# Kernel optimization log

Measured on AMD Instinct MI355X. Metric: run time of the kernel, lower is better.

## Reference

```python
import jax, jax.numpy as jnp
import numpy as np

B, S, D, H, F = 16, 577, 1024, 16, 4096
DH = D // H  # 64
EPS = 1e-6


def _layernorm(x, g, b):
    mu = jnp.mean(x, axis=-1, keepdims=True)
    var = jnp.mean(jnp.square(x - mu), axis=-1, keepdims=True)
    return (x - mu) * jax.lax.rsqrt(var + EPS) * g + b


def setup_inputs() -> dict:
    key = jax.random.key(0)
    ks = jax.random.split(key, 8)
    s = 1.0 / np.sqrt(D)
    sf = 1.0 / np.sqrt(F)
    return {
        "x": jax.random.normal(ks[0], (B, S, D), jnp.float32),
        "ln1_g": jnp.ones((D,), jnp.float32),
        "ln1_b": jnp.zeros((D,), jnp.float32),
        "wq": jax.random.normal(ks[1], (D, D), jnp.float32) * s,
        "bq": jnp.zeros((D,), jnp.float32),
        "wk": jax.random.normal(ks[2], (D, D), jnp.float32) * s,
        "bk": jnp.zeros((D,), jnp.float32),
        "wv": jax.random.normal(ks[3], (D, D), jnp.float32) * s,
        "bv": jnp.zeros((D,), jnp.float32),
        "wo": jax.random.normal(ks[4], (D, D), jnp.float32) * s,
        "bo": jnp.zeros((D,), jnp.float32),
        "ln2_g": jnp.ones((D,), jnp.float32),
        "ln2_b": jnp.zeros((D,), jnp.float32),
        "w1": jax.random.normal(ks[5], (D, F), jnp.float32) * s,
        "b1": jnp.zeros((F,), jnp.float32),
        "w2": jax.random.normal(ks[6], (F, D), jnp.float32) * sf,
        "b2": jnp.zeros((D,), jnp.float32),
    }


def reference(x, ln1_g, ln1_b, wq, bq, wk, bk, wv, bv, wo, bo,
              ln2_g, ln2_b, w1, b1, w2, b2):
    # --- attention sublayer ---
    h = x
    xn = _layernorm(x, ln1_g, ln1_b)
    q = (xn @ wq + bq).reshape(B, S, H, DH).transpose(0, 2, 1, 3)  # b h s d
    k = (xn @ wk + bk).reshape(B, S, H, DH).transpose(0, 2, 1, 3)
    v = (xn @ wv + bv).reshape(B, S, H, DH).transpose(0, 2, 1, 3)
    scores = jnp.einsum('bhqd,bhkd->bhqk', q, k) / np.sqrt(DH)
    probs = jax.nn.softmax(scores, axis=-1)
    ctx = jnp.einsum('bhqk,bhkd->bhqd', probs, v)
    ctx = ctx.transpose(0, 2, 1, 3).reshape(B, S, D)
    attn_out = ctx @ wo + bo  # dropout rate 0 -> mask of ones
    x = attn_out + h
    # --- MLP sublayer ---
    h = x
    xn = _layernorm(x, ln2_g, ln2_b)
    hmid = jax.nn.gelu(xn @ w1 + b1, approximate=False)
    x = (hmid @ w2 + b2) + h
    return x
```

## Files before the change

kernel.cpp:

```cpp
#include <hip/hip_runtime.h>
#include <hip/hip_fp16.h>
#include <math.h>

#define Bn 16
#define Sn 577
#define Dn 1024
#define Hn 16
#define DHn 64
#define Fn 4096
#define NROW (Bn*Sn)
#define EPSf 1e-6f

typedef unsigned short u16;
typedef unsigned int u32;
typedef __attribute__((ext_vector_type(8))) _Float16 f16x8;
typedef __attribute__((ext_vector_type(4))) float f32x4;

__device__ inline u16 f2h(float x) { return __half_as_ushort(__float2half(x)); }

__device__ inline void xcd_swizzle(int& bx, int& by) {
    int gx = gridDim.x;
    int nwg = gx * gridDim.y;
    int n = by * gx + bx;
    if ((nwg & 7) == 0) {
        int cpx = nwg >> 3;
        int w = (n & 7) * cpx + (n >> 3);
        bx = w % gx;
        by = w / gx;
    }
}

__global__ __launch_bounds__(256) void wconv16(const float* __restrict__ W,
                                               u16* __restrict__ T16,
                                               int K, int N) {
    __shared__ float t[32][33];
    int n0 = blockIdx.x * 32, k0 = blockIdx.y * 32;
    int tx = threadIdx.x & 31, ty = threadIdx.x >> 5;
#pragma unroll
    for (int i = 0; i < 4; i++) {
        int kk = ty * 4 + i;
        t[kk][tx] = W[(size_t)(k0 + kk) * N + n0 + tx];
    }
    __syncthreads();
#pragma unroll
    for (int i = 0; i < 4; i++) {
        int nn = ty * 4 + i;
        T16[(size_t)(n0 + nn) * K + k0 + tx] = f2h(t[tx][nn]);
    }
}

__global__ __launch_bounds__(256) void ln_f16(const float* __restrict__ x,
                                              const float* __restrict__ g,
                                              const float* __restrict__ b,
                                              u16* __restrict__ oh) {
    int row = blockIdx.x;
    int tid = threadIdx.x;
    const float* xr = x + (size_t)row * Dn;
    float v[4];
    float s = 0.f;
#pragma unroll
    for (int i = 0; i < 4; i++) { v[i] = xr[tid + i * 256]; s += v[i]; }
    __shared__ float red[256];
    red[tid] = s; __syncthreads();
    for (int o = 128; o > 0; o >>= 1) { if (tid < o) red[tid] += red[tid + o]; __syncthreads(); }
    float mean = red[0] * (1.f / Dn);
    __syncthreads();
    float sq = 0.f;
#pragma unroll
    for (int i = 0; i < 4; i++) { float d = v[i] - mean; sq += d * d; }
    red[tid] = sq; __syncthreads();
    for (int o = 128; o > 0; o >>= 1) { if (tid < o) red[tid] += red[tid + o]; __syncthreads(); }
    float rstd = rsqrtf(red[0] * (1.f / Dn) + EPSf);
#pragma unroll
    for (int i = 0; i < 4; i++) {
        int c = tid + i * 256;
        float y = (v[i] - mean) * rstd * g[c] + b[c];
        oh[(size_t)row * Dn + c] = f2h(y);
    }
}

__global__ __launch_bounds__(256) void ln_kernel(const float* __restrict__ x,
                                                 const float* __restrict__ g,
                                                 const float* __restrict__ b,
                                                 float* __restrict__ out) {
    int row = blockIdx.x;
    int tid = threadIdx.x;
    const float* xr = x + (size_t)row * Dn;
    float v[4];
    float s = 0.f;
#pragma unroll
    for (int i = 0; i < 4; i++) { v[i] = xr[tid + i * 256]; s += v[i]; }
    __shared__ float red[256];
    red[tid] = s; __syncthreads();
    for (int o = 128; o > 0; o >>= 1) { if (tid < o) red[tid] += red[tid + o]; __syncthreads(); }
    float mean = red[0] * (1.f / Dn);
    __syncthreads();
    float sq = 0.f;
#pragma unroll
    for (int i = 0; i < 4; i++) { float d = v[i] - mean; sq += d * d; }
    red[tid] = sq; __syncthreads();
    for (int o = 128; o > 0; o >>= 1) { if (tid < o) red[tid] += red[tid + o]; __syncthreads(); }
    float rstd = rsqrtf(red[0] * (1.f / Dn) + EPSf);
    float* orow = out + (size_t)row * Dn;
#pragma unroll
    for (int i = 0; i < 4; i++) {
        int c = tid + i * 256;
        orow[c] = (v[i] - mean) * rstd * g[c] + b[c];
    }
}

__device__ inline void gld_lds16(const u16* g, u16* l) {
    __builtin_amdgcn_global_load_lds((const __attribute__((address_space(1))) void*)g,
                                     (__attribute__((address_space(3))) void*)l,
                                     16, 0, 0);
}

template<int EPI>
__global__ __launch_bounds__(256, 4) void gemm_1t(
    const u16* __restrict__ A, const u16* __restrict__ B,
    const float* __restrict__ bias, const float* __restrict__ resid,
    float* __restrict__ Cf, u16* __restrict__ Ch,
    int M, int N, int K)
{
    __shared__ u16 lds[2][2][4096];
    const int tid = threadIdx.x;
    const int l = tid & 63, w = tid >> 6;
    const int wr = (w >> 1) * 64, wc = (w & 1) * 64;
    int bx = blockIdx.x, by = blockIdx.y;
    xcd_swizzle(bx, by);
    const int row0 = by * 128, col0 = bx * 128;

    const int sg = w * 2;
    const int tl0 = sg * 16 + (l >> 2);
    const int tl1 = tl0 + 16;
    const int kq0 = (l & 3) ^ ((tl0 >> 1) & 3);
    const int kq1 = (l & 3) ^ ((tl1 >> 1) & 3);
    int ga0 = row0 + tl0; if (ga0 > M - 1) ga0 = M - 1;
    int ga1 = row0 + tl1; if (ga1 > M - 1) ga1 = M - 1;
    int gb0 = col0 + tl0; if (gb0 > N - 1) gb0 = N - 1;
    int gb1 = col0 + tl1; if (gb1 > N - 1) gb1 = N - 1;
    const u16* pA0 = A + (size_t)ga0 * K + kq0 * 8;
    const u16* pA1 = A + (size_t)ga1 * K + kq1 * 8;
    const u16* pB0 = B + (size_t)gb0 * K + kq0 * 8;
    const u16* pB1 = B + (size_t)gb1 * K + kq1 * 8;

    int offA[4], offB[4];
#pragma unroll
    for (int i = 0; i < 4; i++) {
        int ra = wr + i * 16 + (l & 15);
        offA[i] = ra * 32 + (((l >> 4) ^ ((ra >> 1) & 3)) << 3);
        int rb = wc + i * 16 + (l & 15);
        offB[i] = rb * 32 + (((l >> 4) ^ ((rb >> 1) & 3)) << 3);
    }

    f32x4 acc[4][4];
#pragma unroll
    for (int i = 0; i < 4; i++)
#pragma unroll
        for (int j = 0; j < 4; j++)
            acc[i][j] = (f32x4){0.f, 0.f, 0.f, 0.f};

    auto STAGE = [&](int buf, int kk) {
        gld_lds16(pA0 + kk, &lds[buf][0][(sg + 0) * 512]);
        gld_lds16(pA1 + kk, &lds[buf][0][(sg + 1) * 512]);
        gld_lds16(pB0 + kk, &lds[buf][1][(sg + 0) * 512]);
        gld_lds16(pB1 + kk, &lds[buf][1][(sg + 1) * 512]);
    };
    auto COMPUTE = [&](int buf) {
        f16x8 af[4], bf4[4];
#pragma unroll
        for (int i = 0; i < 4; i++) af[i] = *(const f16x8*)(&lds[buf][0][offA[i]]);
#pragma unroll
        for (int j = 0; j < 4; j++) bf4[j] = *(const f16x8*)(&lds[buf][1][offB[j]]);
#pragma unroll
        for (int i = 0; i < 4; i++)
#pragma unroll
            for (int j = 0; j < 4; j++)
                acc[i][j] = __builtin_amdgcn_mfma_f32_16x16x32_f16(af[i], bf4[j], acc[i][j], 0, 0, 0);
    };

    const int nk = K / 32;
    STAGE(0, 0);
    __syncthreads();
    for (int t = 0; t < nk; t += 2) {
        if (t + 1 < nk) STAGE(1, (t + 1) * 32);
        COMPUTE(0);
        __syncthreads();
        if (t + 2 < nk) STAGE(0, (t + 2) * 32);
        COMPUTE(1);
        __syncthreads();
    }

    const int rq = l >> 4;
#pragma unroll
    for (int i = 0; i < 4; i++) {
#pragma unroll
        for (int j = 0; j < 4; j++) {
            int col = col0 + wc + j * 16 + (l & 15);
            float bs = bias[col];
#pragma unroll
            for (int r = 0; r < 4; r++) {
                int rowg = row0 + wr + i * 16 + rq * 4 + r;
                if (rowg >= M) continue;
                float vv = acc[i][j][r] + bs;
                size_t o = (size_t)rowg * N + col;
                if (EPI == 1) {
                    float gl = 0.5f * vv * (1.f + erff(vv * 0.70710678118654752f));
                    Ch[o] = f2h(gl);
                } else if (EPI == 2) {
                    Cf[o] = vv + resid[o];
                } else {
                    Cf[o] = vv;
                }
            }
        }
    }
}

__global__ __launch_bounds__(256, 4) void gemm_qkv(
    const u16* __restrict__ A, const u16* __restrict__ B,
    const float* __restrict__ bq, const float* __restrict__ bk,
    const float* __restrict__ bv,
    u16* __restrict__ qb, u16* __restrict__ kb, u16* __restrict__ vt,
    int M, int N, int K)
{
    __shared__ u16 lds[2][2][4096];
    const int tid = threadIdx.x;
    const int l = tid & 63, w = tid >> 6;
    const int wr = (w >> 1) * 64, wc = (w & 1) * 64;
    int bx = blockIdx.x, by = blockIdx.y;
    xcd_swizzle(bx, by);
    const int row0 = by * 128, col0 = bx * 128;

    const int sg = w * 2;
    const int tl0 = sg * 16 + (l >> 2);
    const int tl1 = tl0 + 16;
    const int kq0 = (l & 3) ^ ((tl0 >> 1) & 3);
    const int kq1 = (l & 3) ^ ((tl1 >> 1) & 3);
    int ga0 = row0 + tl0; if (ga0 > M - 1) ga0 = M - 1;
    int ga1 = row0 + tl1; if (ga1 > M - 1) ga1 = M - 1;
    int gb0 = col0 + tl0; if (gb0 > N - 1) gb0 = N - 1;
    int gb1 = col0 + tl1; if (gb1 > N - 1) gb1 = N - 1;
    const u16* pA0 = A + (size_t)ga0 * K + kq0 * 8;
    const u16* pA1 = A + (size_t)ga1 * K + kq1 * 8;
    const u16* pB0 = B + (size_t)gb0 * K + kq0 * 8;
    const u16* pB1 = B + (size_t)gb1 * K + kq1 * 8;

    int offA[4], offB[4];
#pragma unroll
    for (int i = 0; i < 4; i++) {
        int ra = wr + i * 16 + (l & 15);
        offA[i] = ra * 32 + (((l >> 4) ^ ((ra >> 1) & 3)) << 3);
        int rb = wc + i * 16 + (l & 15);
        offB[i] = rb * 32 + (((l >> 4) ^ ((rb >> 1) & 3)) << 3);
    }

    f32x4 acc[4][4];
#pragma unroll
    for (int i = 0; i < 4; i++)
#pragma unroll
        for (int j = 0; j < 4; j++)
            acc[i][j] = (f32x4){0.f, 0.f, 0.f, 0.f};

    auto STAGE = [&](int buf, int kk) {
        gld_lds16(pA0 + kk, &lds[buf][0][(sg + 0) * 512]);
        gld_lds16(pA1 + kk, &lds[buf][0][(sg + 1) * 512]);
        gld_lds16(pB0 + kk, &lds[buf][1][(sg + 0) * 512]);
        gld_lds16(pB1 + kk, &lds[buf][1][(sg + 1) * 512]);
    };
    auto COMPUTE = [&](int buf) {
        f16x8 af[4], bf4[4];
#pragma unroll
        for (int i = 0; i < 4; i++) af[i] = *(const f16x8*)(&lds[buf][0][offA[i]]);
#pragma unroll
        for (int j = 0; j < 4; j++) bf4[j] = *(const f16x8*)(&lds[buf][1][offB[j]]);
#pragma unroll
        for (int i = 0; i < 4; i++)
#pragma unroll
            for (int j = 0; j < 4; j++)
                acc[i][j] = __builtin_amdgcn_mfma_f32_16x16x32_f16(af[i], bf4[j], acc[i][j], 0, 0, 0);
    };

    const int nk = K / 32;
    STAGE(0, 0);
    __syncthreads();
    for (int t = 0; t < nk; t += 2) {
        if (t + 1 < nk) STAGE(1, (t + 1) * 32);
        COMPUTE(0);
        __syncthreads();
        if (t + 2 < nk) STAGE(0, (t + 2) * 32);
        COMPUTE(1);
        __syncthreads();
    }

    const int rq = l >> 4;
#pragma unroll
    for (int i = 0; i < 4; i++) {
#pragma unroll
        for (int j = 0; j < 4; j++) {
            int col = col0 + wc + j * 16 + (l & 15);
#pragma unroll
            for (int r = 0; r < 4; r++) {
                int rowg = row0 + wr + i * 16 + rq * 4 + r;
                if (rowg >= M) continue;
                float a = acc[i][j][r];
                if (col < 1024) {
                    qb[(size_t)rowg * 1024 + col] = f2h((a + bq[col]) * 0.125f);
                } else if (col < 2048) {
                    int c2 = col - 1024;
                    kb[(size_t)rowg * 1024 + c2] = f2h(a + bk[c2]);
                } else {
                    int c2 = col - 2048;
                    u32 rg = (u32)rowg;
                    u32 bb = rg / 577u;
                    u32 key = rg - bb * 577u;
                    vt[((size_t)((bb * 16 + (c2 >> 6)) * 64 + (c2 & 63))) * 640 + key] =
                        f2h(a + bv[c2]);
                }
            }
        }
    }
}

__global__ __launch_bounds__(256) void flash_mfma(const u16* __restrict__ Qg,
                                                  const u16* __restrict__ Kg,
                                                  const u16* __restrict__ Vt,
                                                  u16* __restrict__ Oh) {
    __shared__ u16 Kl[64 * 64];
    __shared__ u16 Vl[64 * 64];
    __shared__ u16 Pl[64][72];

    int bx = blockIdx.x, by = blockIdx.y;
    xcd_swizzle(bx, by);
    const int qt = bx, bh = by;
    const int b = bh >> 4, h = bh & 15;
    const int tid = threadIdx.x;
    const int l = tid & 63, w = tid >> 6;
    const int q0 = qt * 64;

    int qrow = q0 + w * 16 + (l & 15); if (qrow > 576) qrow = 576;
    const u16* qp = Qg + ((size_t)(b * 577 + qrow)) * 1024 + h * 64 + (l >> 4) * 8;
    f16x8 qf0 = *(const f16x8*)qp;
    f16x8 qf1 = *(const f16x8*)(qp + 32);

    const int swk = ((l & 7) ^ (l >> 3)) * 8;

    f32x4 ctx[4];
#pragma unroll
    for (int d = 0; d < 4; d++) ctx[d] = (f32x4){0.f, 0.f, 0.f, 0.f};
    float m_r[4], l_r[4];
#pragma unroll
    for (int r = 0; r < 4; r++) { m_r[r] = -1e30f; l_r[r] = 0.f; }

    for (int kt = 0; kt < 10; ++kt) {
        const int kb = kt * 64;
#pragma unroll
        for (int c2 = 0; c2 < 2; ++c2) {
            int c = w * 2 + c2;
            int key = kb + c * 8 + (l >> 3); if (key > 576) key = 576;
            const u16* ksrc = Kg + ((size_t)(b * 577 + key)) * 1024 + h * 64 + swk;
            gld_lds16(ksrc, Kl + c * 512);
            int d = c * 8 + (l >> 3);
            const u16* vsrc = Vt + ((size_t)(bh * 64 + d)) * 640 + kb + swk;
            gld_lds16(vsrc, Vl + c * 512);
        }
        __syncthreads();

        f32x4 sc[4];
#pragma unroll
        for (int sub = 0; sub < 4; ++sub) {
            sc[sub] = (f32x4){0.f, 0.f, 0.f, 0.f};
            int rr = sub * 16 + (l & 15);
            int c0 = (l >> 4) ^ (rr & 7);
            int c1 = ((l >> 4) + 4) ^ (rr & 7);
            f16x8 kf0 = *(const f16x8*)(Kl + rr * 64 + c0 * 8);
            f16x8 kf1 = *(const f16x8*)(Kl + rr * 64 + c1 * 8);
            sc[sub] = __builtin_amdgcn_mfma_f32_16x16x32_f16(qf0, kf0, sc[sub], 0, 0, 0);
            sc[sub] = __builtin_amdgcn_mfma_f32_16x16x32_f16(qf1, kf1, sc[sub], 0, 0, 0);
        }

        bool valid[4];
#pragma unroll
        for (int sub = 0; sub < 4; ++sub) valid[sub] = (kb + sub * 16 + (l & 15)) < Sn;

#pragma unroll
        for (int r = 0; r < 4; ++r) {
            float s0 = valid[0] ? sc[0][r] : -1e30f;
            float s1 = valid[1] ? sc[1][r] : -1e30f;
            float s2 = valid[2] ? sc[2][r] : -1e30f;
            float s3 = valid[3] ? sc[3][r] : -1e30f;
            float mx = fmaxf(fmaxf(s0, s1), fmaxf(s2, s3));
            mx = fmaxf(mx, __shfl_xor(mx, 1));
            mx = fmaxf(mx, __shfl_xor(mx, 2));
            mx = fmaxf(mx, __shfl_xor(mx, 4));
            mx = fmaxf(mx, __shfl_xor(mx, 8));
            float mnew = fmaxf(m_r[r], mx);
            float scale = __expf(m_r[r] - mnew);
            float p0 = valid[0] ? __expf(s0 - mnew) : 0.f;
            float p1 = valid[1] ? __expf(s1 - mnew) : 0.f;
            float p2 = valid[2] ? __expf(s2 - mnew) : 0.f;
            float p3 = valid[3] ? __expf(s3 - mnew) : 0.f;
            int prow = w * 16 + (l >> 4) * 4 + r;
            int pcol = l & 15;
            Pl[prow][pcol]      = f2h(p0);
            Pl[prow][pcol + 16] = f2h(p1);
            Pl[prow][pcol + 32] = f2h(p2);
            Pl[prow][pcol + 48] = f2h(p3);
            float rsum = p0 + p1 + p2 + p3;
            rsum += __shfl_xor(rsum, 1);
            rsum += __shfl_xor(rsum, 2);
            rsum += __shfl_xor(rsum, 4);
            rsum += __shfl_xor(rsum, 8);
            l_r[r] = l_r[r] * scale + rsum;
            m_r[r] = mnew;
#pragma unroll
            for (int d = 0; d < 4; ++d) ctx[d][r] *= scale;
        }

#pragma unroll
        for (int ks = 0; ks < 2; ++ks) {
            f16x8 pf = *(const f16x8*)(&Pl[w * 16 + (l & 15)][ks * 32 + (l >> 4) * 8]);
#pragma unroll
            for (int d = 0; d < 4; ++d) {
                int rr = d * 16 + (l & 15);
                int cv = (ks * 4 + (l >> 4)) ^ (rr & 7);
                f16x8 vf = *(const f16x8*)(Vl + rr * 64 + cv * 8);
                ctx[d] = __builtin_amdgcn_mfma_f32_16x16x32_f16(pf, vf, ctx[d], 0, 0, 0);
            }
        }
        __syncthreads();
    }

#pragma unroll
    for (int r = 0; r < 4; ++r) {
        int q = q0 + w * 16 + (l >> 4) * 4 + r;
        if (q >= Sn) continue;
        float inv = 1.f / l_r[r];
#pragma unroll
        for (int d = 0; d < 4; ++d) {
            float t = ctx[d][r] * inv;
            size_t o = ((size_t)(b * 577 + q)) * 1024 + h * 64 + d * 16 + (l & 15);
            Oh[o] = f2h(t);
        }
    }
}

template<int EPI>
__global__ __launch_bounds__(256) void gemm_kernel(const float* __restrict__ A,
                                                   const float* __restrict__ W,
                                                   const float* __restrict__ bias,
                                                   const float* __restrict__ resid,
                                                   float* __restrict__ C,
                                                   int M, int N, int K) {
    const int BM = 64, BN = 64, BK = 16;
    __shared__ float As[BK][BM + 1];
    __shared__ float Ws[BK][BN];
    int tx = threadIdx.x, ty = threadIdx.y;
    int tid = ty * 16 + tx;
    int row0 = blockIdx.y * BM, col0 = blockIdx.x * BN;
    float acc[4][4] = {};
    for (int k0 = 0; k0 < K; k0 += BK) {
#pragma unroll
        for (int i = 0; i < 4; i++) {
            int idx = i * 256 + tid;
            int ar = idx >> 4, ac = idx & 15;
            int grow = row0 + ar;
            As[ac][ar] = (grow < M) ? A[(size_t)grow * K + k0 + ac] : 0.f;
        }
#pragma unroll
        for (int i = 0; i < 4; i++) {
            int idx = i * 256 + tid;
            int wr = idx >> 6, wcc = idx & 63;
            Ws[wr][wcc] = W[(size_t)(k0 + wr) * N + col0 + wcc];
        }
        __syncthreads();
#pragma unroll
        for (int kk = 0; kk < BK; kk++) {
            float a[4], wv[4];
#pragma unroll
            for (int i = 0; i < 4; i++) a[i] = As[kk][ty * 4 + i];
#pragma unroll
            for (int j = 0; j < 4; j++) wv[j] = Ws[kk][tx * 4 + j];
#pragma unroll
            for (int i = 0; i < 4; i++)
#pragma unroll
                for (int j = 0; j < 4; j++)
                    acc[i][j] += a[i] * wv[j];
        }
        __syncthreads();
    }
#pragma unroll
    for (int i = 0; i < 4; i++) {
        int grow = row0 + ty * 4 + i;
        if (grow >= M) continue;
#pragma unroll
        for (int j = 0; j < 4; j++) {
            int gcol = col0 + tx * 4 + j;
            float r = acc[i][j] + bias[gcol];
            if (EPI == 1) r = 0.5f * r * (1.f + erff(r * 0.70710678118654752f));
            if (EPI == 2) r += resid[(size_t)grow * N + gcol];
            C[(size_t)grow * N + gcol] = r;
        }
    }
}

__global__ __launch_bounds__(256) void flash_kernel(const float* __restrict__ Q,
                                                    const float* __restrict__ K,
                                                    const float* __restrict__ V,
                                                    float* __restrict__ Of) {
    __shared__ float Qs[64][68];
    __shared__ float KT[64][68];
    __shared__ float Vs[64][68];
    __shared__ float Ps[64][68];

    int qt = blockIdx.x;
    int bh = blockIdx.y;
    int b = bh >> 4, h = bh & 15;
    int tid = threadIdx.x;
    int tx = tid & 15, ty = tid >> 4;
    size_t base = ((size_t)b * Sn) * Dn + (size_t)h * DHn;
    int q0 = qt * 64;

    {
        int r = tid >> 4;
        int c = (tid & 15) * 4;
#pragma unroll
        for (int i = 0; i < 4; i++) {
            int rr = r + i * 16;
            int gq = q0 + rr;
            float4 val = make_float4(0.f, 0.f, 0.f, 0.f);
            if (gq < Sn) val = *(const float4*)&Q[base + (size_t)gq * Dn + c];
            Qs[rr][c + 0] = val.x * 0.125f;
            Qs[rr][c + 1] = val.y * 0.125f;
            Qs[rr][c + 2] = val.z * 0.125f;
            Qs[rr][c + 3] = val.w * 0.125f;
        }
    }

    float m_r[4], l_r[4], acc[4][4];
#pragma unroll
    for (int i = 0; i < 4; i++) {
        m_r[i] = -1e30f; l_r[i] = 0.f;
#pragma unroll
        for (int j = 0; j < 4; j++) acc[i][j] = 0.f;
    }

    for (int kt = 0; kt < 10; kt++) {
        int kb = kt * 64;
        {
            int r = tid >> 4;
            int c = (tid & 15) * 4;
#pragma unroll
            for (int i = 0; i < 4; i++) {
                int rr = r + i * 16;
                int gk = kb + rr;
                float4 kv = make_float4(0.f, 0.f, 0.f, 0.f);
                float4 vv = make_float4(0.f, 0.f, 0.f, 0.f);
                if (gk < Sn) {
                    kv = *(const float4*)&K[base + (size_t)gk * Dn + c];
                    vv = *(const float4*)&V[base + (size_t)gk * Dn + c];
                }
                KT[c + 0][rr] = kv.x;
                KT[c + 1][rr] = kv.y;
                KT[c + 2][rr] = kv.z;
                KT[c + 3][rr] = kv.w;
                Vs[rr][c + 0] = vv.x;
                Vs[rr][c + 1] = vv.y;
                Vs[rr][c + 2] = vv.z;
                Vs[rr][c + 3] = vv.w;
            }
        }
        __syncthreads();

        float s[4][4] = {};
#pragma unroll
        for (int kk4 = 0; kk4 < 16; kk4++) {
            float4 a4[4], b4[4];
#pragma unroll
            for (int i = 0; i < 4; i++) a4[i] = *(const float4*)&Qs[ty * 4 + i][kk4 * 4];
#pragma unroll
            for (int q = 0; q < 4; q++) b4[q] = *(const float4*)&KT[kk4 * 4 + q][tx * 4];
#pragma unroll
            for (int i = 0; i < 4; i++) {
                float av[4] = {a4[i].x, a4[i].y, a4[i].z, a4[i].w};
#pragma unroll
                for (int q = 0; q < 4; q++) {
                    s[i][0] += av[q] * b4[q].x;
                    s[i][1] += av[q] * b4[q].y;
                    s[i][2] += av[q] * b4[q].z;
                    s[i][3] += av[q] * b4[q].w;
                }
            }
        }

        bool cvalid[4];
#pragma unroll
        for (int j = 0; j < 4; j++) cvalid[j] = (kb + tx * 4 + j) < Sn;
#pragma unroll
        for (int i = 0; i < 4; i++) {
            float lmax = -1e30f;
#pragma unroll
            for (int j = 0; j < 4; j++) if (cvalid[j]) lmax = fmaxf(lmax, s[i][j]);
            lmax = fmaxf(lmax, __shfl_xor(lmax, 1));
            lmax = fmaxf(lmax, __shfl_xor(lmax, 2));
            lmax = fmaxf(lmax, __shfl_xor(lmax, 4));
            lmax = fmaxf(lmax, __shfl_xor(lmax, 8));
            float mnew = fmaxf(m_r[i], lmax);
            float scale = __expf(m_r[i] - mnew);
            float rsum = 0.f;
#pragma unroll
            for (int j = 0; j < 4; j++) {
                float p = cvalid[j] ? __expf(s[i][j] - mnew) : 0.f;
                s[i][j] = p;
                rsum += p;
            }
            rsum += __shfl_xor(rsum, 1);
            rsum += __shfl_xor(rsum, 2);
            rsum += __shfl_xor(rsum, 4);
            rsum += __shfl_xor(rsum, 8);
            l_r[i] = l_r[i] * scale + rsum;
            m_r[i] = mnew;
#pragma unroll
            for (int j = 0; j < 4; j++) acc[i][j] *= scale;
        }

#pragma unroll
        for (int i = 0; i < 4; i++)
#pragma unroll
            for (int j = 0; j < 4; j++)
                Ps[ty * 4 + i][tx * 4 + j] = s[i][j];
        __syncthreads();

#pragma unroll
        for (int kk4 = 0; kk4 < 16; kk4++) {
            float4 a4[4], b4[4];
#pragma unroll
            for (int i = 0; i < 4; i++) a4[i] = *(const float4*)&Ps[ty * 4 + i][kk4 * 4];
#pragma unroll
            for (int q = 0; q < 4; q++) b4[q] = *(const float4*)&Vs[kk4 * 4 + q][tx * 4];
#pragma unroll
            for (int i = 0; i < 4; i++) {
                float av[4] = {a4[i].x, a4[i].y, a4[i].z, a4[i].w};
#pragma unroll
                for (int q = 0; q < 4; q++) {
                    acc[i][0] += av[q] * b4[q].x;
                    acc[i][1] += av[q] * b4[q].y;
                    acc[i][2] += av[q] * b4[q].z;
                    acc[i][3] += av[q] * b4[q].w;
                }
            }
        }
        __syncthreads();
    }

#pragma unroll
    for (int i = 0; i < 4; i++) {
        int gq = q0 + ty * 4 + i;
        if (gq >= Sn) continue;
        float inv = 1.f / l_r[i];
#pragma unroll
        for (int j = 0; j < 4; j++)
            Of[base + (size_t)gq * Dn + tx * 4 + j] = acc[i][j] * inv;
    }
}

extern "C" void kernel_launch(void* const* d_in, const int* in_sizes, int n_in,
                              void* d_out, int out_size, void* d_ws, size_t ws_size,
                              hipStream_t stream) {
    const float* x    = (const float*)d_in[0];
    const float* ln1g = (const float*)d_in[1];
    const float* ln1b = (const float*)d_in[2];
    const float* wq   = (const float*)d_in[3];
    const float* bq   = (const float*)d_in[4];
    const float* wk   = (const float*)d_in[5];
    const float* bk   = (const float*)d_in[6];
    const float* wv   = (const float*)d_in[7];
    const float* bv   = (const float*)d_in[8];
    const float* wo   = (const float*)d_in[9];
    const float* bo   = (const float*)d_in[10];
    const float* ln2g = (const float*)d_in[11];
    const float* ln2b = (const float*)d_in[12];
    const float* w1   = (const float*)d_in[13];
    const float* b1   = (const float*)d_in[14];
    const float* w2   = (const float*)d_in[15];
    const float* b2   = (const float*)d_in[16];
    float* out = (float*)d_out;
    char* ws = (char*)d_ws;

    const size_t WHALF_D = (size_t)1024 * 1024 * 2;
    const size_t WHALF_F = (size_t)4096 * 1024 * 2;
    const size_t HALF_XN = (size_t)NROW * 1024 * 2;
    const size_t BASE_A  = 8 * WHALF_D + 4 * WHALF_F;
    const size_t NEED = BASE_A + 10 * HALF_XN;
    const size_t VT_BYTES = (size_t)Bn * Hn * 64 * 640 * 2;

    if (ws_size >= NEED) {
        u16* wqkvT = (u16*)(ws);
        u16* woT   = (u16*)(ws + 6 * WHALF_D);
        u16* w1T   = (u16*)(ws + 8 * WHALF_D);
        u16* w2T   = (u16*)(ws + 8 * WHALF_D + 2 * WHALF_F);
        char* S = ws + BASE_A;
        u16* xn_h  = (u16*)(S + 0 * HALF_XN);
        u16* qb    = (u16*)(S + 2 * HALF_XN);
        u16* kb2   = (u16*)(S + 3 * HALF_XN);
        u16* vtb   = (u16*)(S + 4 * HALF_XN);
        u16* ctx_h = (u16*)(S + 8 * HALF_XN);
        u16* xn2_h = (u16*)(S + 9 * HALF_XN);
        u16* hm_h  = (u16*)(S + 0 * HALF_XN);

        wconv16<<<dim3(32, 32), 256, 0, stream>>>(wq, wqkvT,                   1024, 1024);
        wconv16<<<dim3(32, 32), 256, 0, stream>>>(wk, wqkvT + 1024 * 1024,     1024, 1024);
        wconv16<<<dim3(32, 32), 256, 0, stream>>>(wv, wqkvT + 2 * 1024 * 1024, 1024, 1024);
        wconv16<<<dim3(32, 32), 256, 0, stream>>>(wo, woT, 1024, 1024);
        wconv16<<<dim3(128, 32), 256, 0, stream>>>(w1, w1T, 1024, 4096);
        wconv16<<<dim3(32, 128), 256, 0, stream>>>(w2, w2T, 4096, 1024);

        hipMemsetAsync(vtb, 0, VT_BYTES, stream);

        ln_f16<<<NROW, 256, 0, stream>>>(x, ln1g, ln1b, xn_h);
        gemm_qkv<<<dim3(24, 73), 256, 0, stream>>>(xn_h, wqkvT, bq, bk, bv,
                                                   qb, kb2, vtb, NROW, 3072, 1024);
        flash_mfma<<<dim3(10, Bn * Hn), 256, 0, stream>>>(qb, kb2, vtb, ctx_h);
        gemm_1t<2><<<dim3(8, 73), 256, 0, stream>>>(
            ctx_h, woT, bo, x, out, nullptr, NROW, 1024, 1024);
        ln_f16<<<NROW, 256, 0, stream>>>(out, ln2g, ln2b, xn2_h);
        gemm_1t<1><<<dim3(32, 73), 256, 0, stream>>>(
            xn2_h, w1T, b1, nullptr, nullptr, hm_h, NROW, 4096, 1024);
        gemm_1t<2><<<dim3(8, 73), 256, 0, stream>>>(
            hm_h, w2T, b2, out, out, nullptr, NROW, 1024, 4096);
    } else {
        const size_t SZ = (size_t)NROW * Dn * sizeof(float);
        float* qbuf  = (float*)(ws);
        float* kbuf  = (float*)(ws + SZ);
        float* vbuf  = (float*)(ws + 2 * SZ);
        float* hmid  = (float*)(ws);
        float* xnbuf = (float*)(ws + 4 * SZ);
        float* ctx   = (float*)(ws + 5 * SZ);
        float* x1    = (float*)(ws + 6 * SZ);
        dim3 blk2(16, 16);
        dim3 gD(Dn / 64, (NROW + 63) / 64);
        dim3 gF(Fn / 64, (NROW + 63) / 64);
        ln_kernel<<<NROW, 256, 0, stream>>>(x, ln1g, ln1b, xnbuf);
        gemm_kernel<0><<<gD, blk2, 0, stream>>>(xnbuf, wq, bq, nullptr, qbuf, NROW, Dn, Dn);
        gemm_kernel<0><<<gD, blk2, 0, stream>>>(xnbuf, wk, bk, nullptr, kbuf, NROW, Dn, Dn);
        gemm_kernel<0><<<gD, blk2, 0, stream>>>(xnbuf, wv, bv, nullptr, vbuf, NROW, Dn, Dn);
        flash_kernel<<<dim3(10, Bn * Hn), 256, 0, stream>>>(qbuf, kbuf, vbuf, ctx);
        gemm_kernel<2><<<gD, blk2, 0, stream>>>(ctx, wo, bo, x, x1, NROW, Dn, Dn);
        ln_kernel<<<NROW, 256, 0, stream>>>(x1, ln2g, ln2b, xnbuf);
        gemm_kernel<1><<<gF, blk2, 0, stream>>>(xnbuf, w1, b1, nullptr, hmid, NROW, Fn, Dn);
        gemm_kernel<2><<<gD, blk2, 0, stream>>>(hmid, w2, b2, x1, out, NROW, Dn, Fn);
    }
}
```

Measured before the change: 566.7 us.

## Double GEMM K-tile depth to 64 with 8-way XOR LDS swizzle

The fp16 MFMA GEMM now stages 64-wide K slices instead of 32 per pipeline step. Each thread issues four global-to-LDS loads per operand, and LDS reads use an 8-chunk XOR swizzle keyed on row&7. This halves the number of barriers and loop iterations per K and gives each step more MFMA work between syncs. In exchange LDS use doubles to 64KB per block and launch bounds drop to 2 blocks per CU, which lowers occupancy.

```diff
diff --git a/kernel.cpp b/kernel.cpp
--- a/kernel.cpp
+++ b/kernel.cpp
@@ -116,13 +116,13 @@
 }
 
 template<int EPI>
-__global__ __launch_bounds__(256, 4) void gemm_1t(
+__global__ __launch_bounds__(256, 2) void gemm_1t(
     const u16* __restrict__ A, const u16* __restrict__ B,
     const float* __restrict__ bias, const float* __restrict__ resid,
     float* __restrict__ Cf, u16* __restrict__ Ch,
     int M, int N, int K)
 {
-    __shared__ u16 lds[2][2][4096];
+    __shared__ u16 lds[2][2][128 * 64];
     const int tid = threadIdx.x;
     const int l = tid & 63, w = tid >> 6;
     const int wr = (w >> 1) * 64, wc = (w & 1) * 64;
@@ -130,28 +130,27 @@
     xcd_swizzle(bx, by);
     const int row0 = by * 128, col0 = bx * 128;
 
-    const int sg = w * 2;
-    const int tl0 = sg * 16 + (l >> 2);
-    const int tl1 = tl0 + 16;
-    const int kq0 = (l & 3) ^ ((tl0 >> 1) & 3);
-    const int kq1 = (l & 3) ^ ((tl1 >> 1) & 3);
-    int ga0 = row0 + tl0; if (ga0 > M - 1) ga0 = M - 1;
-    int ga1 = row0 + tl1; if (ga1 > M - 1) ga1 = M - 1;
-    int gb0 = col0 + tl0; if (gb0 > N - 1) gb0 = N - 1;
-    int gb1 = col0 + tl1; if (gb1 > N - 1) gb1 = N - 1;
-    const u16* pA0 = A + (size_t)ga0 * K + kq0 * 8;
-    const u16* pA1 = A + (size_t)ga1 * K + kq1 * 8;
-    const u16* pB0 = B + (size_t)gb0 * K + kq0 * 8;
-    const u16* pB1 = B + (size_t)gb1 * K + kq1 * 8;
-
-    int offA[4], offB[4];
+    const int srow = w * 32 + (l >> 3);
+    const int skq  = ((l & 7) ^ (l >> 3)) * 8;
+    const u16* pA[4];
+    const u16* pB[4];
+#pragma unroll
+    for (int g = 0; g < 4; g++) {
+        int ra = row0 + srow + g * 8; if (ra > M - 1) ra = M - 1;
+        int rb = col0 + srow + g * 8; if (rb > N - 1) rb = N - 1;
+        pA[g] = A + (size_t)ra * K + skq;
+        pB[g] = B + (size_t)rb * K + skq;
+    }
+
+    int offA[4], r7A[4], offB[4], r7B[4];
 #pragma unroll
     for (int i = 0; i < 4; i++) {
         int ra = wr + i * 16 + (l & 15);
-        offA[i] = ra * 32 + (((l >> 4) ^ ((ra >> 1) & 3)) << 3);
+        offA[i] = ra * 64; r7A[i] = ra & 7;
         int rb = wc + i * 16 + (l & 15);
-        offB[i] = rb * 32 + (((l >> 4) ^ ((rb >> 1) & 3)) << 3);
-    }
+        offB[i] = rb * 64; r7B[i] = rb & 7;
+    }
+    const int cgrp = l >> 4;
 
     f32x4 acc[4][4];
 #pragma unroll
@@ -161,32 +160,39 @@
             acc[i][j] = (f32x4){0.f, 0.f, 0.f, 0.f};
 
     auto STAGE = [&](int buf, int kk) {
-        gld_lds16(pA0 + kk, &lds[buf][0][(sg + 0) * 512]);
-        gld_lds16(pA1 + kk, &lds[buf][0][(sg + 1) * 512]);
-        gld_lds16(pB0 + kk, &lds[buf][1][(sg + 0) * 512]);
-        gld_lds16(pB1 + kk, &lds[buf][1][(sg + 1) * 512]);
+#pragma unroll
+        for (int g = 0; g < 4; g++)
+            gld_lds16(pA[g] + kk, &lds[buf][0][(w * 32 + g * 8) * 64]);
+#pragma unroll
+        for (int g = 0; g < 4; g++)
+            gld_lds16(pB[g] + kk, &lds[buf][1][(w * 32 + g * 8) * 64]);
     };
     auto COMPUTE = [&](int buf) {
-        f16x8 af[4], bf4[4];
-#pragma unroll
-        for (int i = 0; i < 4; i++) af[i] = *(const f16x8*)(&lds[buf][0][offA[i]]);
-#pragma unroll
-        for (int j = 0; j < 4; j++) bf4[j] = *(const f16x8*)(&lds[buf][1][offB[j]]);
-#pragma unroll
-        for (int i = 0; i < 4; i++)
+#pragma unroll
+        for (int ks = 0; ks < 2; ks++) {
+            f16x8 af[4], bf4[4];
+#pragma unroll
+            for (int i = 0; i < 4; i++)
+                af[i] = *(const f16x8*)(&lds[buf][0][offA[i] + (((ks * 4 + cgrp) ^ r7A[i]) << 3)]);
 #pragma unroll
             for (int j = 0; j < 4; j++)
-                acc[i][j] = __builtin_amdgcn_mfma_f32_16x16x32_f16(af[i], bf4[j], acc[i][j], 0, 0, 0);
+                bf4[j] = *(const f16x8*)(&lds[buf][1][offB[j] + (((ks * 4 + cgrp) ^ r7B[j]) << 3)]);
+#pragma unroll
+            for (int i = 0; i < 4; i++)
+#pragma unroll
+                for (int j = 0; j < 4; j++)
+                    acc[i][j] = __builtin_amdgcn_mfma_f32_16x16x32_f16(af[i], bf4[j], acc[i][j], 0, 0, 0);
+        }
     };
 
-    const int nk = K / 32;
+    const int nk = K / 64;
     STAGE(0, 0);
     __syncthreads();
     for (int t = 0; t < nk; t += 2) {
-        if (t + 1 < nk) STAGE(1, (t + 1) * 32);
+        if (t + 1 < nk) STAGE(1, (t + 1) * 64);
         COMPUTE(0);
         __syncthreads();
-        if (t + 2 < nk) STAGE(0, (t + 2) * 32);
+        if (t + 2 < nk) STAGE(0, (t + 2) * 64);
         COMPUTE(1);
         __syncthreads();
     }
```

Measured after the change: 637.8 us. 1.13x slower.
